# Kernel tuning notes

Hardware: AMD Instinct MI355X
Metric: run time of the kernel (lower is better)

Reference implementation:

```python
import math
import jax, jax.numpy as jnp
import numpy as np

N, T, C, V = 16, 2048, 512, 500


def setup_inputs() -> dict:
    key = jax.random.key(0)
    k1, k2, k3 = jax.random.split(key, 3)
    x = jax.random.normal(k1, (N, T, C), dtype=jnp.float32)
    x_lens = jax.random.randint(k2, (N,), 1, T + 1).astype(jnp.int64)
    # stand-in for CTC log-posteriors; randn makes the blank channel pass the
    ctc_output = jax.random.normal(k3, (N, T, V), dtype=jnp.float32)
    return {"x": x, "x_lens": x_lens, "ctc_output": ctc_output, "blank_id": 0}


def reference(x, x_lens, ctc_output, blank_id):
    # x: [N, T, C], x_lens: [N], ctc_output: [N, T, V]
    n, t_max, _ = x.shape
    t = jnp.arange(t_max)
    padding_mask = t[None, :] >= x_lens[:, None]                      # [N, T]
    non_blank = (ctc_output[:, :, blank_id] < math.log(0.9)) & (~padding_mask)
    lens_fr = non_blank.sum(axis=1)                                   # [N]
    # stable argsort of ~mask: kept frame indices first, in original order
    order = jnp.argsort(~non_blank, axis=1, stable=True)              # [N, T]
    x_fr = jnp.take_along_axis(x, order[:, :, None], axis=1)          # [N, T, C]
    valid = t[None, :] < lens_fr[:, None]
    x_fr = jnp.where(valid[:, :, None], x_fr, jnp.zeros((), x.dtype))  # zero pad like pad_sequence
    t_prime = int(jnp.max(lens_fr))  # concrete (eager) -> [N, T', C] like torch
    return x_fr[:, :t_prime, :], lens_fr
```

## Files before the change

kernel.cpp:

```cpp
#include <hip/hip_runtime.h>
#include <hip/hip_bf16.h>


typedef float f32x4 __attribute__((ext_vector_type(4)));

__global__ void compact_kernel(const float* __restrict__ ctc,
                               const void* __restrict__ x_lens_raw,
                               const int* __restrict__ blank_id_p,
                               int T, int V, int N,
                               int* __restrict__ idx,
                               int* __restrict__ lens,
                               float* __restrict__ lens_out) {
    const int n    = blockIdx.x;
    const int tid  = threadIdx.x;
    const int lane = tid & 63;
    const int wid  = tid >> 6;
    const int ITERS = (T + 1023) >> 10;
    const int NCHUNK = ITERS * 16;

    __shared__ int wcnt[64];
    __shared__ int pfx[65];

    const int* li = (const int*)x_lens_raw;
    long long L;
    if (N > 1 && li[1] == 0) {
        L = ((const long long*)x_lens_raw)[n];
    } else {
        L = (long long)li[n];
    }

    const int blank = *blank_id_p;
    const float thr = -0.10536052f;

    unsigned long long bal[4];
    #pragma unroll
    for (int j = 0; j < 4; ++j) bal[j] = 0ull;

    for (int j = 0; j < ITERS; ++j) {
        int t = (j << 10) + tid;
        bool keep = false;
        if (t < T) {
            float v = ctc[((long long)n * T + t) * V + blank];
            keep = (v < thr) && ((long long)t < L);
        }
        bal[j] = __ballot(keep);
        if (lane == 0) wcnt[j * 16 + wid] = __popcll(bal[j]);
    }
    __syncthreads();

    if (tid == 0) {
        int acc = 0;
        for (int c = 0; c < NCHUNK; ++c) { pfx[c] = acc; acc += wcnt[c]; }
        pfx[NCHUNK] = acc;
        lens[n] = acc;
        __builtin_nontemporal_store((float)acc, lens_out + n);
    }
    __syncthreads();

    int* my_idx = idx + (long long)n * T;
    for (int j = 0; j < ITERS; ++j) {
        int t = (j << 10) + tid;
        unsigned long long b = bal[j];
        if (b & (1ull << lane)) {
            int rank = __popcll(b & ((1ull << lane) - 1ull));
            my_idx[pfx[j * 16 + wid] + rank] = t;
        }
    }
}

__global__ __launch_bounds__(256) void gather_kernel(
        const f32x4* __restrict__ x,
        const int* __restrict__ idx,
        const int* __restrict__ lens,
        f32x4* __restrict__ out,
        int Tp, int T, int f4_per_seq) {
    const int n   = blockIdx.y;
    const int gid = blockIdx.x * 256 + threadIdx.x;
    if (gid >= f4_per_seq) return;
    const int p  = gid >> 7;
    const int c4 = gid & 127;

    f32x4 v = (f32x4)0.f;
    if (p < lens[n]) {
        int tsrc = idx[n * T + p];
        v = x[((long long)(n * T + tsrc) << 7) + c4];
    }
    __builtin_nontemporal_store(v, out + ((long long)n * Tp << 7) + gid);
}

extern "C" void kernel_launch(void* const* d_in, const int* in_sizes, int n_in,
                              void* d_out, int out_size, void* d_ws, size_t ws_size,
                              hipStream_t stream) {
    const float* x        = (const float*)d_in[0];
    const void*  x_lens   = d_in[1];
    const float* ctc      = (const float*)d_in[2];
    const int*   blank_id = (const int*)d_in[3];

    const int N = in_sizes[1];
    const int C = 512;
    const int V = 500;
    const int T = in_sizes[0] / (N * C);
    const int Tp = (out_size - N) / (N * C);

    int* idx  = (int*)d_ws;
    int* lens = idx + (long long)N * T;

    float* out      = (float*)d_out;
    float* lens_out = out + (long long)N * Tp * C;

    compact_kernel<<<N, 1024, 0, stream>>>(ctc, x_lens, blank_id, T, V, N,
                                           idx, lens, lens_out);

    const int f4_per_seq = Tp * (C / 4);
    dim3 ggrid((f4_per_seq + 255) / 256, N);
    gather_kernel<<<ggrid, 256, 0, stream>>>((const f32x4*)x, idx, lens,
                                             (f32x4*)out, Tp, T, f4_per_seq);
}
```

Measured before the change: 16.83 us.

## Split compaction across many blocks with per-segment counts and gather-side prefix search

Replaces the one-block-per-sequence compaction kernel with a grid of 128-thread blocks, one per 128-frame segment. Each block writes its kept indices locally compacted within its segment slot plus a count. The gather kernel now computes the per-sequence prefix over segment counts in shared memory, binary-searches it for each output row, writes lens, and uses nontemporal loads for x. This spreads the strided blank-column reads over many CUs, at the cost of redundant prefix scans in every gather block and a fixed pfx[33] size that assumes T is at most 4096.

```diff
diff --git a/kernel.cpp b/kernel.cpp
--- a/kernel.cpp
+++ b/kernel.cpp
@@ -4,86 +4,78 @@
 
 typedef float f32x4 __attribute__((ext_vector_type(4)));
 
-__global__ void compact_kernel(const float* __restrict__ ctc,
-                               const void* __restrict__ x_lens_raw,
-                               const int* __restrict__ blank_id_p,
-                               int T, int V, int N,
-                               int* __restrict__ idx,
-                               int* __restrict__ lens,
-                               float* __restrict__ lens_out) {
-    const int n    = blockIdx.x;
+__global__ __launch_bounds__(128) void mask_emit_kernel(
+        const float* __restrict__ ctc,
+        const void* __restrict__ x_lens_raw,
+        const int* __restrict__ blank_id_p,
+        int N, int T, int V,
+        int* __restrict__ seg,
+        int* __restrict__ cnt) {
+    const int n    = blockIdx.y;
+    const int b    = blockIdx.x;
     const int tid  = threadIdx.x;
     const int lane = tid & 63;
-    const int wid  = tid >> 6;
-    const int ITERS = (T + 1023) >> 10;
-    const int NCHUNK = ITERS * 16;
-
-    __shared__ int wcnt[64];
-    __shared__ int pfx[65];
+    const int w    = tid >> 6;
+    const int B    = gridDim.x;
+    const int t    = b * 128 + tid;
 
     const int* li = (const int*)x_lens_raw;
-    long long L;
-    if (N > 1 && li[1] == 0) {
-        L = ((const long long*)x_lens_raw)[n];
-    } else {
-        L = (long long)li[n];
+    long long L = (N > 1 && li[1] == 0) ? ((const long long*)x_lens_raw)[n]
+                                        : (long long)li[n];
+
+    bool keep = false;
+    if (t < T) {
+        float v = ctc[((long long)n * T + t) * V + *blank_id_p];
+        keep = (v < -0.10536052f) && ((long long)t < L);
     }
+    unsigned long long bal = __ballot(keep);
 
-    const int blank = *blank_id_p;
-    const float thr = -0.10536052f;
-
-    unsigned long long bal[4];
-    #pragma unroll
-    for (int j = 0; j < 4; ++j) bal[j] = 0ull;
-
-    for (int j = 0; j < ITERS; ++j) {
-        int t = (j << 10) + tid;
-        bool keep = false;
-        if (t < T) {
-            float v = ctc[((long long)n * T + t) * V + blank];
-            keep = (v < thr) && ((long long)t < L);
-        }
-        bal[j] = __ballot(keep);
-        if (lane == 0) wcnt[j * 16 + wid] = __popcll(bal[j]);
-    }
+    __shared__ int w0cnt;
+    if (w == 0 && lane == 0) w0cnt = __popcll(bal);
     __syncthreads();
 
-    if (tid == 0) {
-        int acc = 0;
-        for (int c = 0; c < NCHUNK; ++c) { pfx[c] = acc; acc += wcnt[c]; }
-        pfx[NCHUNK] = acc;
-        lens[n] = acc;
-        __builtin_nontemporal_store((float)acc, lens_out + n);
+    const int base = (w == 0) ? 0 : w0cnt;
+    if (keep) {
+        int rank = __popcll(bal & ((1ull << lane) - 1ull));
+        seg[n * T + b * 128 + base + rank] = t;
     }
-    __syncthreads();
-
-    int* my_idx = idx + (long long)n * T;
-    for (int j = 0; j < ITERS; ++j) {
-        int t = (j << 10) + tid;
-        unsigned long long b = bal[j];
-        if (b & (1ull << lane)) {
-            int rank = __popcll(b & ((1ull << lane) - 1ull));
-            my_idx[pfx[j * 16 + wid] + rank] = t;
-        }
-    }
+    if (w == 1 && lane == 0) cnt[n * B + b] = w0cnt + __popcll(bal);
 }
 
 __global__ __launch_bounds__(256) void gather_kernel(
         const f32x4* __restrict__ x,
-        const int* __restrict__ idx,
-        const int* __restrict__ lens,
+        const int* __restrict__ seg,
+        const int* __restrict__ cnt,
         f32x4* __restrict__ out,
-        int Tp, int T, int f4_per_seq) {
-    const int n   = blockIdx.y;
+        float* __restrict__ lens_out,
+        int Tp, int T, int B, int f4_per_seq) {
+    const int n = blockIdx.y;
+    __shared__ int pfx[33];
+
+    if (threadIdx.x == 0) {
+        int acc = 0;
+        const int* c = cnt + n * B;
+        for (int i = 0; i < B; ++i) { pfx[i] = acc; acc += c[i]; }
+        pfx[B] = acc;
+    }
+    __syncthreads();
+    const int lens = pfx[B];
+    if (blockIdx.x == 0 && threadIdx.x == 0) lens_out[n] = (float)lens;
+
     const int gid = blockIdx.x * 256 + threadIdx.x;
     if (gid >= f4_per_seq) return;
     const int p  = gid >> 7;
     const int c4 = gid & 127;
 
     f32x4 v = (f32x4)0.f;
-    if (p < lens[n]) {
-        int tsrc = idx[n * T + p];
-        v = x[((long long)(n * T + tsrc) << 7) + c4];
+    if (p < lens) {
+        int lo = 0, hi = B;
+        while (hi - lo > 1) {
+            int mid = (lo + hi) >> 1;
+            if (pfx[mid] <= p) lo = mid; else hi = mid;
+        }
+        int tsrc = seg[n * T + lo * 128 + (p - pfx[lo])];
+        v = __builtin_nontemporal_load(x + ((long long)(n * T + tsrc) << 7) + c4);
     }
     __builtin_nontemporal_store(v, out + ((long long)n * Tp << 7) + gid);
 }
@@ -101,18 +93,21 @@
     const int V = 500;
     const int T = in_sizes[0] / (N * C);
     const int Tp = (out_size - N) / (N * C);
+    const int B = (T + 127) / 128;
 
-    int* idx  = (int*)d_ws;
-    int* lens = idx + (long long)N * T;
+    int* seg = (int*)d_ws;
+    int* cnt = seg + (long long)N * T;
 
     float* out      = (float*)d_out;
     float* lens_out = out + (long long)N * Tp * C;
 
-    compact_kernel<<<N, 1024, 0, stream>>>(ctc, x_lens, blank_id, T, V, N,
-                                           idx, lens, lens_out);
+    dim3 mgrid(B, N);
+    mask_emit_kernel<<<mgrid, 128, 0, stream>>>(ctc, x_lens, blank_id,
+                                                N, T, V, seg, cnt);
 
     const int f4_per_seq = Tp * (C / 4);
     dim3 ggrid((f4_per_seq + 255) / 256, N);
-    gather_kernel<<<ggrid, 256, 0, stream>>>((const f32x4*)x, idx, lens,
-                                             (f32x4*)out, Tp, T, f4_per_seq);
+    gather_kernel<<<ggrid, 256, 0, stream>>>((const f32x4*)x, seg, cnt,
+                                             (f32x4*)out, lens_out,
+                                             Tp, T, B, f4_per_seq);
 }
```

Measured after the change: 20.38 us. 21.1% more time.
